# Kernel optimization log

Hardware: AMD Instinct MI355X
Metric: run time of the kernel (lower is better)

## Reference

```python
import jax, jax.numpy as jnp
import numpy as np

CANVAS_W = 1024.0
CANVAS_H = 1024.0
EPS = 1e-8
GOLDEN = 1.618
ALIGN_THRESH = 5.0


def _mse(p, t):
    return jnp.mean((p - t) ** 2)


def _smooth_l1(p, t):
    d = jnp.abs(p - t)
    return jnp.mean(jnp.where(d < 1.0, 0.5 * d * d, d - 0.5))


def setup_inputs() -> dict:
    key = jax.random.key(0)
    k1, k2, k3, k4 = jax.random.split(key, 4)
    B, N, D = 64, 256, 6
    return {
        "predicted_noise": jax.random.normal(k1, (B, N, D), dtype=jnp.float32),
        "target_noise": jax.random.normal(k2, (B, N, D), dtype=jnp.float32),
        "predicted_layout": jax.random.normal(k3, (B, N, D), dtype=jnp.float32),
        "target_layout": jax.random.normal(k4, (B, N, D), dtype=jnp.float32),
        "element_mask": jnp.ones((B, N), dtype=jnp.float32),
    }


def _iou_loss(pred, target):
    # boxes are (x, y, w, h)
    px1, py1 = pred[..., 0], pred[..., 1]
    px2, py2 = px1 + pred[..., 2], py1 + pred[..., 3]
    tx1, ty1 = target[..., 0], target[..., 1]
    tx2, ty2 = tx1 + target[..., 2], ty1 + target[..., 3]
    inter = jnp.maximum(jnp.minimum(px2, tx2) - jnp.maximum(px1, tx1), 0.0) * \
            jnp.maximum(jnp.minimum(py2, ty2) - jnp.maximum(py1, ty1), 0.0)
    pa = pred[..., 2] * pred[..., 3]
    ta = target[..., 2] * target[..., 3]
    iou = inter / (pa + ta - inter + EPS)
    return jnp.mean(1.0 - iou)


def _loss(predicted_noise, target_noise, predicted_layout, target_layout, element_mask):
    B, N, _ = predicted_noise.shape
    mask3 = element_mask[..., None]  # [B,N,1]
    pn = predicted_noise * mask3
    tn = target_noise * mask3
    pl = predicted_layout * mask3
    tl = target_layout * mask3

    npairs = N * (N - 1) / 2.0
    tri = jnp.triu(jnp.ones((N, N), dtype=pl.dtype), k=1)  # i<j pair mask
    pair_valid = element_mask[:, :, None] * element_mask[:, None, :]  # [B,N,N]

    # ---- noise loss (SmoothL1) ----
    noise_loss = _smooth_l1(pn, tn)

    # ---- position loss: MSE + 0.5*IoU ----
    position_loss = _mse(pl[..., :4], tl[..., :4]) + 0.5 * _iou_loss(pl[..., :4], tl[..., :4])

    # ---- layer loss: MSE + 0.3*pairwise ranking BCE ----
    p_layer, t_layer = pl[..., 4], tl[..., 4]
    diff = p_layer[:, None, :] - p_layer[:, :, None]          # [b,i,j] = p_j - p_i
    y = (t_layer[:, :, None] < t_layer[:, None, :]).astype(pl.dtype)
    # BCE(sigmoid(diff), y): -log sigmoid(d)=softplus(-d); torch clamps log terms at 100
    bce = y * jnp.minimum(jax.nn.softplus(-diff), 100.0) + \
          (1.0 - y) * jnp.minimum(jax.nn.softplus(diff), 100.0)
    ranking = jnp.sum(bce * tri) / (B * npairs)
    layer_loss = _mse(p_layer, t_layer) + 0.3 * ranking

    # ---- confidence loss ----
    confidence_loss = _mse(pl[..., 5], tl[..., 5])

    # ---- aesthetic loss ----
    aspect = pl[..., 2] / (pl[..., 3] + EPS)
    golden = jnp.mean(jnp.abs(aspect - GOLDEN))
    areas = pl[..., 2] * pl[..., 3] * element_mask
    size_harm = jnp.mean(jnp.std(areas, axis=1, ddof=1)) / (jnp.mean(areas) + EPS)
    cx = (pl[..., 0] + pl[..., 2] / 2) * element_mask
    cy = (pl[..., 1] + pl[..., 3] / 2) * element_mask
    valid_count = jnp.sum(element_mask, axis=1, keepdims=True)  # [B,1]
    # NOTE: faithful to original broadcasting ([B] / [B,1] -> [B,B])
    ocx = jnp.sum(cx, axis=1) / (valid_count + EPS)
    ocy = jnp.sum(cy, axis=1) / (valid_count + EPS)
    balance = jnp.mean(jnp.abs(ocx - CANVAS_W / 2) / (CANVAS_W / 2) +
                       jnp.abs(ocy - CANVAS_H / 2) / (CANVAS_H / 2))
    aesthetic_loss = 0.1 * golden + 0.2 * size_harm + 0.15 * balance

    # ---- overlap loss (pairwise) ----
    x1, y1, w, h = pl[..., 0], pl[..., 1], pl[..., 2], pl[..., 3]
    x2, y2 = x1 + w, y1 + h
    iw = jnp.maximum(jnp.minimum(x2[:, :, None], x2[:, None, :]) -
                     jnp.maximum(x1[:, :, None], x1[:, None, :]), 0.0)
    ih = jnp.maximum(jnp.minimum(y2[:, :, None], y2[:, None, :]) -
                     jnp.maximum(y1[:, :, None], y1[:, None, :]), 0.0)
    area = w * h
    min_area = jnp.minimum(area[:, :, None], area[:, None, :])
    overlap_ratio = (iw * ih) / (min_area + EPS) * pair_valid
    overlap_loss = jnp.sum(overlap_ratio * tri) / (B * npairs)

    # ---- alignment loss (6 edge types, pairwise) ----
    edges = jnp.stack([x1, x2, y1, y2, x1 + w / 2, y1 + h / 2], axis=0)  # [6,B,N]
    dist = jnp.abs(edges[:, :, :, None] - edges[:, :, None, :])          # [6,B,N,N]
    pen = jnp.where(dist < ALIGN_THRESH, dist / ALIGN_THRESH, 0.0) * pair_valid[None]
    alignment_loss = jnp.sum(pen * tri) / (B * 6.0 * npairs)

    total = (noise_loss + 1.0 * position_loss + 0.5 * layer_loss +
             0.3 * confidence_loss + 0.2 * aesthetic_loss +
             0.8 * overlap_loss + 0.4 * alignment_loss)
    return total


def reference(predicted_noise, target_noise, predicted_layout, target_layout, element_mask):
    return _loss(predicted_noise, target_noise, predicted_layout, target_layout, element_mask)
```

## Files before the change

### kernel.cpp

```cpp
#include <hip/hip_runtime.h>
#include <math.h>

#define NB 64
#define NN 256
#define NPAIRS 32640.0f
#define EPSF 1e-8f

#define PB(q) ((q) * 64)
#define PW(q) (704 + (q) * 1024)

__device__ __forceinline__ float block_sum(float v, float* sred) {
    const int tid = threadIdx.x;
    #pragma unroll
    for (int off = 32; off > 0; off >>= 1) v += __shfl_down(v, off, 64);
    __syncthreads();
    if ((tid & 63) == 0) sred[tid >> 6] = v;
    __syncthreads();
    return sred[0] + sred[1] + sred[2] + sred[3];
}

__device__ __forceinline__ void block_sum3(float a, float b, float c, float* sred,
                                           float& ra, float& rb, float& rc) {
    const int tid = threadIdx.x;
    #pragma unroll
    for (int off = 32; off > 0; off >>= 1) {
        a += __shfl_down(a, off, 64);
        b += __shfl_down(b, off, 64);
        c += __shfl_down(c, off, 64);
    }
    __syncthreads();
    if ((tid & 63) == 0) {
        const int w = tid >> 6;
        sred[w] = a; sred[4 + w] = b; sred[8 + w] = c;
    }
    __syncthreads();
    ra = sred[0] + sred[1] + sred[2]  + sred[3];
    rb = sred[4] + sred[5] + sred[6]  + sred[7];
    rc = sred[8] + sred[9] + sred[10] + sred[11];
}

__device__ __forceinline__ float wave_sum(float v) {
    #pragma unroll
    for (int off = 32; off > 0; off >>= 1) v += __shfl_down(v, off, 64);
    return v;
}

__global__ __launch_bounds__(256) void loss_main(
    const float* __restrict__ pn, const float* __restrict__ tn,
    const float* __restrict__ pl, const float* __restrict__ tl,
    const float* __restrict__ mask, float* __restrict__ ws)
{
    __shared__ float4 sA[NN], sB[NN];
    __shared__ float2 sC[NN];
    __shared__ float sred[12];

    const int b     = blockIdx.x >> 4;
    const int chunk = blockIdx.x & 15;
    const int i     = threadIdx.x;
    const int e     = b * NN + i;
    const float m   = mask[e];

    const float2* pl2 = (const float2*)pl;
    const float2* tl2 = (const float2*)tl;
    const int r2 = e * 3;
    const float2 pla = pl2[r2 + 0], plb = pl2[r2 + 1], plc = pl2[r2 + 2];
    const float2 tlc = tl2[r2 + 2];

    const float p0 = pla.x * m, p1 = pla.y * m,
                p2 = plb.x * m, p3 = plb.y * m,
                p4 = plc.x * m, p5 = plc.y * m;
    const float t4 = tlc.x * m, t5 = tlc.y * m;

    const float x2v = p0 + p2, y2v = p1 + p3;
    const float areav = p2 * p3;
    const float cxe = p0 + 0.5f * p2, cye = p1 + 0.5f * p3;

    sA[i] = make_float4(p0, p1, x2v, y2v);
    sB[i] = make_float4(cxe, cye, areav, p4);
    sC[i] = make_float2(t4, m);
    __syncthreads();

    float rank = 0.f, ovl = 0.f, aln = 0.f;
    const int dd0 = chunk * 8 + 1;
    #pragma unroll
    for (int k = 0; k < 8; ++k) {
        const int dd = dd0 + k;
        int j = (i + dd) & 255;
        if (dd == 128 && i >= 128) continue;
        float4 aj = sA[j];
        float4 bj = sB[j];
        float2 cj = sC[j];
        float pv = m * cj.y;
        float ow = fmaxf(fminf(x2v, aj.z) - fmaxf(p0, aj.x), 0.f);
        float oh = fmaxf(fminf(y2v, aj.w) - fmaxf(p1, aj.y), 0.f);
        ovl += ow * oh * pv * __builtin_amdgcn_rcpf(fminf(areav, bj.z) + EPSF);
        float pen = 0.f, d;
        d = fabsf(p0  - aj.x); pen += (d < 5.f) ? d : 0.f;
        d = fabsf(x2v - aj.z); pen += (d < 5.f) ? d : 0.f;
        d = fabsf(p1  - aj.y); pen += (d < 5.f) ? d : 0.f;
        d = fabsf(y2v - aj.w); pen += (d < 5.f) ? d : 0.f;
        d = fabsf(cxe - bj.x); pen += (d < 5.f) ? d : 0.f;
        d = fabsf(cye - bj.y); pen += (d < 5.f) ? d : 0.f;
        aln += pen * (0.2f * pv);
        bool ilt = (i < j);
        float dlo = ilt ? (bj.w - p4) : (p4 - bj.w);
        bool ylt  = ilt ? (t4 < cj.x) : (cj.x < t4);
        float z   = ylt ? -dlo : dlo;
        float sp  = __logf(1.f + __expf(-fabsf(z))) + fmaxf(z, 0.f);
        rank += fminf(sp, 100.f);
    }

    {
        float sr, so, sa;
        block_sum3(rank, ovl, aln, sred, sr, so, sa);
        if (i == 0) {
            ws[PW(0) + blockIdx.x] = sr;
            ws[PW(1) + blockIdx.x] = so;
            ws[PW(2) + blockIdx.x] = sa;
        }
    }

    float v = 0.f;
    bool have = true;
    switch (chunk) {
    case 0: {
        const float2* pn2 = (const float2*)pn;
        const float2* tn2 = (const float2*)tn;
        float noise = 0.f;
        #pragma unroll
        for (int k = 0; k < 3; ++k) {
            float2 a = pn2[r2 + k], bb = tn2[r2 + k];
            float d0 = fabsf(a.x * m - bb.x * m);
            float d1 = fabsf(a.y * m - bb.y * m);
            noise += (d0 < 1.f) ? 0.5f * d0 * d0 : d0 - 0.5f;
            noise += (d1 < 1.f) ? 0.5f * d1 * d1 : d1 - 0.5f;
        }
        v = noise;
        break; }
    case 1: {
        const float2 tla = tl2[r2 + 0], tlb = tl2[r2 + 1];
        const float t0 = tla.x * m, t1 = tla.y * m,
                    t2 = tlb.x * m, t3 = tlb.y * m;
        v = (p0 - t0) * (p0 - t0) + (p1 - t1) * (p1 - t1)
          + (p2 - t2) * (p2 - t2) + (p3 - t3) * (p3 - t3);
        break; }
    case 2: {
        const float2 tla = tl2[r2 + 0], tlb = tl2[r2 + 1];
        const float t0 = tla.x * m, t1 = tla.y * m,
                    t2 = tlb.x * m, t3 = tlb.y * m;
        const float tx2 = t0 + t2, ty2 = t1 + t3;
        float iw = fmaxf(fminf(x2v, tx2) - fmaxf(p0, t0), 0.f);
        float ih = fmaxf(fminf(y2v, ty2) - fmaxf(p1, t1), 0.f);
        float inter = iw * ih;
        v = 1.f - inter / (areav + t2 * t3 - inter + EPSF);
        break; }
    case 3: v = (p4 - t4) * (p4 - t4); break;
    case 4: v = (p5 - t5) * (p5 - t5); break;
    case 5: v = fabsf(p2 / (p3 + EPSF) - 1.618f); break;
    case 6: v = areav * m; break;
    case 7: { float a = areav * m; v = a * a; break; }
    case 8: v = cxe * m; break;
    case 9: v = cye * m; break;
    case 10: v = m; break;
    default: have = false; break;
    }
    if (have) {
        float s = block_sum(v, sred);
        if (i == 0) ws[PB(chunk) + b] = s;
    }
}

__global__ __launch_bounds__(64) void loss_final(
    const float* __restrict__ ws, float* __restrict__ out)
{
    const int t = threadIdx.x;

    float v_noise = ws[PB(0) + t];
    float v_pos   = ws[PB(1) + t];
    float v_iou   = ws[PB(2) + t];
    float v_lm    = ws[PB(3) + t];
    float v_cf    = ws[PB(4) + t];
    float v_go    = ws[PB(5) + t];
    float v_ar    = ws[PB(6) + t];
    float a2      = ws[PB(7) + t];
    float v_cx    = ws[PB(8) + t];
    float v_cy    = ws[PB(9) + t];
    float v_vc    = ws[PB(10) + t];
    float var   = (a2 - v_ar * v_ar * (1.f / 256.f)) * (1.f / 255.f);
    float v_std = sqrtf(fmaxf(var, 0.f));

    float v_rank = 0.f, v_ovl = 0.f, v_aln = 0.f;
    #pragma unroll
    for (int k = 0; k < 16; ++k) {
        v_rank += ws[PW(0) + k * 64 + t];
        v_ovl  += ws[PW(1) + k * 64 + t];
        v_aln  += ws[PW(2) + k * 64 + t];
    }

    float inv = 1.f / (v_vc + EPSF);
    float v_bal = 0.f;
    for (int j = 0; j < NB; ++j) {
        float cxj = __shfl(v_cx, j, 64);
        float cyj = __shfl(v_cy, j, 64);
        v_bal += fabsf(cxj * inv - 512.f) * (1.f / 512.f)
               + fabsf(cyj * inv - 512.f) * (1.f / 512.f);
    }

    float S_noise = wave_sum(v_noise);
    float S_pos   = wave_sum(v_pos);
    float S_iou   = wave_sum(v_iou);
    float S_lm    = wave_sum(v_lm);
    float S_cf    = wave_sum(v_cf);
    float S_go    = wave_sum(v_go);
    float S_ar    = wave_sum(v_ar);
    float S_std   = wave_sum(v_std);
    float S_bal   = wave_sum(v_bal);
    float S_rank  = wave_sum(v_rank);
    float S_ovl   = wave_sum(v_ovl);
    float S_aln   = wave_sum(v_aln);

    if (t == 0) {
        const float BN = 64.f * 256.f;
        float noise_loss = S_noise / (BN * 6.f);
        float position   = S_pos / (BN * 4.f) + 0.5f * (S_iou / BN);
        float layer      = S_lm / BN + 0.3f * (S_rank / (64.f * NPAIRS));
        float conf       = S_cf / BN;
        float golden     = S_go / BN;
        float size_harm  = (S_std / 64.f) / (S_ar / BN + EPSF);
        float balance    = S_bal / 4096.f;
        float aes        = 0.1f * golden + 0.2f * size_harm + 0.15f * balance;
        float ovl        = S_ovl / (64.f * NPAIRS);
        float aln        = S_aln / (64.f * 6.f * NPAIRS);
        out[0] = noise_loss + position + 0.5f * layer + 0.3f * conf
               + 0.2f * aes + 0.8f * ovl + 0.4f * aln;
    }
}

extern "C" void kernel_launch(void* const* d_in, const int* in_sizes, int n_in,
                              void* d_out, int out_size, void* d_ws, size_t ws_size,
                              hipStream_t stream) {
    const float* pn   = (const float*)d_in[0];
    const float* tn   = (const float*)d_in[1];
    const float* pl   = (const float*)d_in[2];
    const float* tl   = (const float*)d_in[3];
    const float* mask = (const float*)d_in[4];
    float* ws  = (float*)d_ws;
    float* out = (float*)d_out;
    hipLaunchKernelGGL(loss_main, dim3(1024), dim3(256), 0, stream,
                       pn, tn, pl, tl, mask, ws);
    hipLaunchKernelGGL(loss_final, dim3(1), dim3(64), 0, stream, ws, out);
}
```

Baseline: 72.15 us.

## Merge main and final kernels into one cooperative launch with a grid sync

Measured after the change: 109.9 us. +52.4%, slower.

```diff
diff --git a/kernel.cpp b/kernel.cpp
--- a/kernel.cpp
+++ b/kernel.cpp
@@ -1,43 +1,14 @@
 #include <hip/hip_runtime.h>
+#include <hip/hip_cooperative_groups.h>
 #include <math.h>
+
+namespace cg = cooperative_groups;
 
 #define NB 64
 #define NN 256
 #define NPAIRS 32640.0f
 #define EPSF 1e-8f
 
-#define PB(q) ((q) * 64)
-#define PW(q) (704 + (q) * 1024)
-
-__device__ __forceinline__ float block_sum(float v, float* sred) {
-    const int tid = threadIdx.x;
-    #pragma unroll
-    for (int off = 32; off > 0; off >>= 1) v += __shfl_down(v, off, 64);
-    __syncthreads();
-    if ((tid & 63) == 0) sred[tid >> 6] = v;
-    __syncthreads();
-    return sred[0] + sred[1] + sred[2] + sred[3];
-}
-
-__device__ __forceinline__ void block_sum3(float a, float b, float c, float* sred,
-                                           float& ra, float& rb, float& rc) {
-    const int tid = threadIdx.x;
-    #pragma unroll
-    for (int off = 32; off > 0; off >>= 1) {
-        a += __shfl_down(a, off, 64);
-        b += __shfl_down(b, off, 64);
-        c += __shfl_down(c, off, 64);
-    }
-    __syncthreads();
-    if ((tid & 63) == 0) {
-        const int w = tid >> 6;
-        sred[w] = a; sred[4 + w] = b; sred[8 + w] = c;
-    }
-    __syncthreads();
-    ra = sred[0] + sred[1] + sred[2]  + sred[3];
-    rb = sred[4] + sred[5] + sred[6]  + sred[7];
-    rc = sred[8] + sred[9] + sred[10] + sred[11];
-}
 
 __device__ __forceinline__ float wave_sum(float v) {
     #pragma unroll
@@ -45,20 +16,22 @@
     return v;
 }
 
-__global__ __launch_bounds__(256) void loss_main(
+__global__ __launch_bounds__(512) void loss_coop(
     const float* __restrict__ pn, const float* __restrict__ tn,
     const float* __restrict__ pl, const float* __restrict__ tl,
-    const float* __restrict__ mask, float* __restrict__ ws)
+    const float* __restrict__ mask, float* __restrict__ ws,
+    float* __restrict__ out)
 {
     __shared__ float4 sA[NN], sB[NN];
     __shared__ float2 sC[NN];
-    __shared__ float sred[12];
-
-    const int b     = blockIdx.x >> 4;
-    const int chunk = blockIdx.x & 15;
-    const int i     = threadIdx.x;
-    const int e     = b * NN + i;
-    const float m   = mask[e];
+    __shared__ float sred[14 * 8];
+
+    const int b    = blockIdx.x;
+    const int tid  = threadIdx.x;
+    const int i    = tid & 255;
+    const int half = tid >> 8;
+    const int e    = b * NN + i;
+    const float m  = mask[e];
 
     const float2* pl2 = (const float2*)pl;
     const float2* tl2 = (const float2*)tl;
@@ -75,15 +48,52 @@
     const float areav = p2 * p3;
     const float cxe = p0 + 0.5f * p2, cye = p1 + 0.5f * p3;
 
-    sA[i] = make_float4(p0, p1, x2v, y2v);
-    sB[i] = make_float4(cxe, cye, areav, p4);
-    sC[i] = make_float2(t4, m);
+    if (half == 0) {
+        sA[i] = make_float4(p0, p1, x2v, y2v);
+        sB[i] = make_float4(cxe, cye, areav, p4);
+        sC[i] = make_float2(t4, m);
+    }
     __syncthreads();
 
+    float d_noise = 0.f, d_pos = 0.f, d_iou = 0.f, d_lm = 0.f, d_cf = 0.f,
+          d_go = 0.f, d_ar = 0.f, d_a2 = 0.f, d_cx = 0.f, d_cy = 0.f, d_vc = 0.f;
+    if (half == 0) {
+        const float2* pn2 = (const float2*)pn;
+        const float2* tn2 = (const float2*)tn;
+        float noise = 0.f;
+        #pragma unroll
+        for (int k = 0; k < 3; ++k) {
+            float2 a = pn2[r2 + k], bb = tn2[r2 + k];
+            float d0 = fabsf(a.x * m - bb.x * m);
+            float d1 = fabsf(a.y * m - bb.y * m);
+            noise += (d0 < 1.f) ? 0.5f * d0 * d0 : d0 - 0.5f;
+            noise += (d1 < 1.f) ? 0.5f * d1 * d1 : d1 - 0.5f;
+        }
+        d_noise = noise;
+        const float2 tla = tl2[r2 + 0], tlb = tl2[r2 + 1];
+        const float t0 = tla.x * m, t1 = tla.y * m,
+                    t2 = tlb.x * m, t3 = tlb.y * m;
+        d_pos = (p0 - t0) * (p0 - t0) + (p1 - t1) * (p1 - t1)
+              + (p2 - t2) * (p2 - t2) + (p3 - t3) * (p3 - t3);
+        const float tx2 = t0 + t2, ty2 = t1 + t3;
+        float iw = fmaxf(fminf(x2v, tx2) - fmaxf(p0, t0), 0.f);
+        float ih = fmaxf(fminf(y2v, ty2) - fmaxf(p1, t1), 0.f);
+        float inter = iw * ih;
+        d_iou = 1.f - inter / (areav + t2 * t3 - inter + EPSF);
+        d_lm  = (p4 - t4) * (p4 - t4);
+        d_cf  = (p5 - t5) * (p5 - t5);
+        d_go  = fabsf(p2 / (p3 + EPSF) - 1.618f);
+        d_ar  = areav * m;
+        d_a2  = d_ar * d_ar;
+        d_cx  = cxe * m;
+        d_cy  = cye * m;
+        d_vc  = m;
+    }
+
     float rank = 0.f, ovl = 0.f, aln = 0.f;
-    const int dd0 = chunk * 8 + 1;
-    #pragma unroll
-    for (int k = 0; k < 8; ++k) {
+    const int dd0 = half * 64 + 1;
+    #pragma unroll 8
+    for (int k = 0; k < 64; ++k) {
         const int dd = dd0 + k;
         int j = (i + dd) & 255;
         if (dd == 128 && i >= 128) continue;
@@ -111,91 +121,47 @@
     }
 
     {
-        float sr, so, sa;
-        block_sum3(rank, ovl, aln, sred, sr, so, sa);
-        if (i == 0) {
-            ws[PW(0) + blockIdx.x] = sr;
-            ws[PW(1) + blockIdx.x] = so;
-            ws[PW(2) + blockIdx.x] = sa;
+        float r[14] = {rank, ovl, aln, d_noise, d_pos, d_iou, d_lm, d_cf,
+                       d_go, d_ar, d_a2, d_cx, d_cy, d_vc};
+        const int w = tid >> 6;
+        #pragma unroll
+        for (int q = 0; q < 14; ++q) {
+            float v = r[q];
+            #pragma unroll
+            for (int off = 32; off > 0; off >>= 1) v += __shfl_down(v, off, 64);
+            if ((tid & 63) == 0) sred[q * 8 + w] = v;
         }
-    }
-
-    float v = 0.f;
-    bool have = true;
-    switch (chunk) {
-    case 0: {
-        const float2* pn2 = (const float2*)pn;
-        const float2* tn2 = (const float2*)tn;
-        float noise = 0.f;
-        #pragma unroll
-        for (int k = 0; k < 3; ++k) {
-            float2 a = pn2[r2 + k], bb = tn2[r2 + k];
-            float d0 = fabsf(a.x * m - bb.x * m);
-            float d1 = fabsf(a.y * m - bb.y * m);
-            noise += (d0 < 1.f) ? 0.5f * d0 * d0 : d0 - 0.5f;
-            noise += (d1 < 1.f) ? 0.5f * d1 * d1 : d1 - 0.5f;
+        __syncthreads();
+        if (tid < 14) {
+            float s = 0.f;
+            #pragma unroll
+            for (int ww = 0; ww < 8; ++ww) s += sred[tid * 8 + ww];
+            ws[b * 16 + tid] = s;
         }
-        v = noise;
-        break; }
-    case 1: {
-        const float2 tla = tl2[r2 + 0], tlb = tl2[r2 + 1];
-        const float t0 = tla.x * m, t1 = tla.y * m,
-                    t2 = tlb.x * m, t3 = tlb.y * m;
-        v = (p0 - t0) * (p0 - t0) + (p1 - t1) * (p1 - t1)
-          + (p2 - t2) * (p2 - t2) + (p3 - t3) * (p3 - t3);
-        break; }
-    case 2: {
-        const float2 tla = tl2[r2 + 0], tlb = tl2[r2 + 1];
-        const float t0 = tla.x * m, t1 = tla.y * m,
-                    t2 = tlb.x * m, t3 = tlb.y * m;
-        const float tx2 = t0 + t2, ty2 = t1 + t3;
-        float iw = fmaxf(fminf(x2v, tx2) - fmaxf(p0, t0), 0.f);
-        float ih = fmaxf(fminf(y2v, ty2) - fmaxf(p1, t1), 0.f);
-        float inter = iw * ih;
-        v = 1.f - inter / (areav + t2 * t3 - inter + EPSF);
-        break; }
-    case 3: v = (p4 - t4) * (p4 - t4); break;
-    case 4: v = (p5 - t5) * (p5 - t5); break;
-    case 5: v = fabsf(p2 / (p3 + EPSF) - 1.618f); break;
-    case 6: v = areav * m; break;
-    case 7: { float a = areav * m; v = a * a; break; }
-    case 8: v = cxe * m; break;
-    case 9: v = cye * m; break;
-    case 10: v = m; break;
-    default: have = false; break;
-    }
-    if (have) {
-        float s = block_sum(v, sred);
-        if (i == 0) ws[PB(chunk) + b] = s;
-    }
-}
-
-__global__ __launch_bounds__(64) void loss_final(
-    const float* __restrict__ ws, float* __restrict__ out)
-{
-    const int t = threadIdx.x;
-
-    float v_noise = ws[PB(0) + t];
-    float v_pos   = ws[PB(1) + t];
-    float v_iou   = ws[PB(2) + t];
-    float v_lm    = ws[PB(3) + t];
-    float v_cf    = ws[PB(4) + t];
-    float v_go    = ws[PB(5) + t];
-    float v_ar    = ws[PB(6) + t];
-    float a2      = ws[PB(7) + t];
-    float v_cx    = ws[PB(8) + t];
-    float v_cy    = ws[PB(9) + t];
-    float v_vc    = ws[PB(10) + t];
+    }
+
+    cg::this_grid().sync();
+
+    if (blockIdx.x != 0) return;
+    const int t = tid;
+    if (t >= 64) return;
+
+    float v_rank  = ws[t * 16 + 0];
+    float v_ovl   = ws[t * 16 + 1];
+    float v_aln   = ws[t * 16 + 2];
+    float v_noise = ws[t * 16 + 3];
+    float v_pos   = ws[t * 16 + 4];
+    float v_iou   = ws[t * 16 + 5];
+    float v_lm    = ws[t * 16 + 6];
+    float v_cf    = ws[t * 16 + 7];
+    float v_go    = ws[t * 16 + 8];
+    float v_ar    = ws[t * 16 + 9];
+    float a2      = ws[t * 16 + 10];
+    float v_cx    = ws[t * 16 + 11];
+    float v_cy    = ws[t * 16 + 12];
+    float v_vc    = ws[t * 16 + 13];
     float var   = (a2 - v_ar * v_ar * (1.f / 256.f)) * (1.f / 255.f);
     float v_std = sqrtf(fmaxf(var, 0.f));
-
-    float v_rank = 0.f, v_ovl = 0.f, v_aln = 0.f;
-    #pragma unroll
-    for (int k = 0; k < 16; ++k) {
-        v_rank += ws[PW(0) + k * 64 + t];
-        v_ovl  += ws[PW(1) + k * 64 + t];
-        v_aln  += ws[PW(2) + k * 64 + t];
-    }
 
     float inv = 1.f / (v_vc + EPSF);
     float v_bal = 0.f;
@@ -246,7 +212,8 @@
     const float* mask = (const float*)d_in[4];
     float* ws  = (float*)d_ws;
     float* out = (float*)d_out;
-    hipLaunchKernelGGL(loss_main, dim3(1024), dim3(256), 0, stream,
-                       pn, tn, pl, tl, mask, ws);
-    hipLaunchKernelGGL(loss_final, dim3(1), dim3(64), 0, stream, ws, out);
+    void* args[] = { (void*)&pn, (void*)&tn, (void*)&pl, (void*)&tl,
+                     (void*)&mask, (void*)&ws, (void*)&out };
+    hipLaunchCooperativeKernel((const void*)loss_coop, dim3(NB), dim3(512),
+                               args, 0, stream);
 }
```
